# Kernel tuning notes

Measured on AMD Instinct MI355X. Metric: run time of the kernel, lower is better.

The kernel has to match this reference:

```python
import jax, jax.numpy as jnp
from jax import lax
import numpy as np

RANK, OUT_C, IN_C, K = 4, 128, 128, 3
B, H, W = 32, 56, 56


def setup_inputs() -> dict:
    key = jax.random.key(0)
    ks = jax.random.split(key, 7)
    x = jax.random.normal(ks[0], (B, IN_C, H, W), dtype=jnp.float32)
    # init_weights_normal per rank -> plain gaussian with fan-in scaling
    w = jax.random.normal(ks[1], (RANK, OUT_C, IN_C, K, K), dtype=jnp.float32) / np.sqrt(IN_C * K * K)
    cw_row = jax.random.normal(ks[2], (RANK, H, 1), dtype=jnp.float32) * 0.1
    cw_col = jax.random.normal(ks[3], (RANK, 1, W), dtype=jnp.float32) * 0.1
    b_row = jax.random.normal(ks[4], (1, 1, H, 1), dtype=jnp.float32) * 0.01
    b_col = jax.random.normal(ks[5], (1, 1, 1, W), dtype=jnp.float32) * 0.01
    b = jax.random.normal(ks[6], (1, OUT_C, 1, 1), dtype=jnp.float32) * 0.01
    return {"x": x, "w": w, "cw_row": cw_row, "cw_col": cw_col,
            "b_row": b_row, "b_col": b_col, "b": b}


def reference(x, w, cw_row, cw_col, b_row, b_col, b):
    # lrlc_nan branch: one big conv with rank*out_channels filters,
    # then per-spatial-location low-rank combining weights.
    rank, oc, ic, kh, kw = w.shape
    w_flat = w.reshape(rank * oc, ic, kh, kw)
    convs = lax.conv_general_dilated(
        x, w_flat,
        window_strides=(1, 1),
        padding=((1, 1), (1, 1)),
        dimension_numbers=("NCHW", "OIHW", "NCHW"),
    )  # [B, rank*oc, H, W]
    bsz = x.shape[0]
    hh, ww = convs.shape[2], convs.shape[3]
    convs = convs.reshape(bsz, rank, oc, hh, ww)
    # softmax over rank of per-location combining weights [rank, H, W]
    cw = jax.nn.softmax(cw_row + cw_col, axis=0)
    out = jnp.einsum("bkcxy,kxy->bcxy", convs, cw)
    # bias_pd: per-channel + per-row + per-col biases
    out = out + b + b_col + b_row
    return out
```

## Files before the change

### kernel.cpp

```cpp
#include <hip/hip_runtime.h>

#define NB 32
#define NC 128
#define NH 56
#define NW 56
#define HP 58
#define WP 58
#define KK 1152
#define NPOS 3136
#define XT_BYTES (NB * HP * WP * NC * 2)
#define AW_OFF XT_BYTES

typedef __attribute__((ext_vector_type(8))) short s16x8;
typedef __attribute__((ext_vector_type(4))) float f32x4;
typedef unsigned int u32;

__device__ __forceinline__ unsigned short f2bf(float f) {
    union { float f; unsigned int u; } v; v.f = f;
    unsigned int u = v.u + 0x7fffu + ((v.u >> 16) & 1u);
    return (unsigned short)(u >> 16);
}

__device__ __forceinline__ void gld16(const void* g, void* l) {
    __builtin_amdgcn_global_load_lds(
        (const __attribute__((address_space(1))) u32*)g,
        (__attribute__((address_space(3))) u32*)l, 16, 0, 0);
}

__global__ void k_xpose(const float* __restrict__ x, unsigned short* __restrict__ xt) {
    __shared__ unsigned short tile[128 * 57];
    int blk = blockIdx.x;
    int b = blk / NH, y = blk % NH;
    int tid = threadIdx.x;
    const float* xb = x + (size_t)b * (NC * NPOS) + y * NW;
#pragma unroll
    for (int p = 0; p < 7; ++p) {
        int idx = p * 256 + tid;
        int c = idx / 14, i = idx - c * 14;
        float4 v = *(const float4*)(xb + c * NPOS + i * 4);
        unsigned short* tp = &tile[c * 57 + i * 4];
        tp[0] = f2bf(v.x); tp[1] = f2bf(v.y); tp[2] = f2bf(v.z); tp[3] = f2bf(v.w);
    }
    __syncthreads();
    unsigned short* xrow = xt + ((size_t)(b * HP + y + 1) * WP + 1) * NC;
#pragma unroll
    for (int p = 0; p < 4; ++p) {
        int idx = p * 256 + tid;
        if (idx < 896) {
            int xp = idx >> 4, cgi = idx & 15;
            s16x8 v8;
#pragma unroll
            for (int j = 0; j < 8; ++j)
                v8[j] = (short)tile[(cgi * 8 + j) * 57 + xp];
            *(s16x8*)(xrow + xp * NC + cgi * 8) = v8;
        }
    }
    if (tid < 128) {
        xt[((size_t)(b * HP + y + 1) * WP + 0) * NC + tid] = 0;
        xt[((size_t)(b * HP + y + 1) * WP + 57) * NC + tid] = 0;
    }
    if (y == 0) {
        unsigned short* r0 = xt + (size_t)(b * HP + 0) * WP * NC;
        for (int i = tid; i < WP * NC; i += 256) r0[i] = 0;
    }
    if (y == 55) {
        unsigned short* r57 = xt + (size_t)(b * HP + 57) * WP * NC;
        for (int i = tid; i < WP * NC; i += 256) r57[i] = 0;
    }
}

__global__ void k_wconv(const float* __restrict__ w, unsigned short* __restrict__ aw) {
    int idx = blockIdx.x * 256 + threadIdx.x;
    if (idx >= 512 * KK) return;
    int j = idx & 7, lane = (idx >> 3) & 63, mt = (idx >> 9) & 31, s = idx >> 14;
    int m = mt * 16 + (lane & 15);
    int kg = s * 32 + (lane >> 4) * 8 + j;
    int g = kg >> 7, ic = kg & 127;
    aw[idx] = f2bf(w[(m * 128 + ic) * 9 + g]);
}

__global__ void __launch_bounds__(512, 2) k_main(
    const unsigned short* __restrict__ xt, const unsigned short* __restrict__ aw,
    const float* __restrict__ cwr, const float* __restrict__ cwc,
    const float* __restrict__ brow, const float* __restrict__ bcol,
    const float* __restrict__ bch, float* __restrict__ out) {
    __shared__ __align__(16) unsigned char ldsB[28672];

    const int tid = threadIdx.x;
    const int lane = tid & 63;
    const int wv = tid >> 6;
    const int l15 = lane & 15, quad = lane >> 4;
    const int blk = blockIdx.x;
    const int b = blk / 28;
    const int tile0 = (blk - b * 28) * 112;

    const unsigned char* gB0 = nullptr;
    const unsigned char* gB1 = nullptr;
    if (wv < 7) {
#pragma unroll
        for (int h = 0; h < 2; ++h) {
            int row = wv * 16 + h * 8 + (lane >> 3);
            int pos = tile0 + row;
            int yy = pos / 56, xx = pos - yy * 56;
            const unsigned char* p = (const unsigned char*)xt
                + (size_t)b * (HP * WP * NC * 2)
                + ((yy + 1) * WP + (xx + 1)) * (NC * 2)
                + (((lane & 7) ^ (lane >> 3)) * 16);
            if (h == 0) gB0 = p; else gB1 = p;
        }
    }

    const unsigned char* gA = (const unsigned char*)aw + wv * 1024 + lane * 16;

    s16x8 Areg[2][2][4];
    f32x4 acc[4][7] = {};

    auto aload = [&](int st, int set) {
#pragma unroll
        for (int kk = 0; kk < 2; ++kk)
#pragma unroll
            for (int r = 0; r < 4; ++r)
                Areg[set][kk][r] = *(const s16x8*)(gA + (((2 * st + kk) * 32 + r * 8) << 10));
    };

    auto bstage = [&](int st, int pbuf) {
        if (wv < 7) {
            int g = st >> 1;
            int dy = (g * 11) >> 5;
            int dx = g - dy * 3;
            int off = ((dy - 1) * WP + (dx - 1)) * (NC * 2) + (st & 1) * 128;
            unsigned char* L = ldsB + pbuf * 14336 + wv * 2048;
            gld16(gB0 + off, L);
            gld16(gB1 + off, L + 1024);
        }
    };

    bstage(0, 0);
    aload(0, 0);
    __syncthreads();

    for (int st = 0; st < 18; ++st) {
        const int cur = st & 1;
        if (st < 17) {
            bstage(st + 1, cur ^ 1);
            aload(st + 1, cur ^ 1);
        }
        const unsigned char* L = ldsB + cur * 14336;
#pragma unroll
        for (int kk = 0; kk < 2; ++kk) {
            s16x8 bf[7];
#pragma unroll
            for (int t = 0; t < 7; ++t)
                bf[t] = *(const s16x8*)(L + (t * 16 + l15) * 128
                                          + (((kk * 4 + quad) ^ (l15 & 7)) * 16));
#pragma unroll
            for (int r = 0; r < 4; ++r)
#pragma unroll
                for (int t = 0; t < 7; ++t)
                    acc[r][t] = __builtin_amdgcn_mfma_f32_16x16x32_bf16(
                        Areg[cur][kk][r], bf[t], acc[r][t], 0, 0, 0);
        }
        __syncthreads();
    }

#pragma unroll
    for (int t = 0; t < 7; ++t) {
        int pos = tile0 + t * 16 + l15;
        int yy = pos / 56, xx = pos - yy * 56;
        float v0 = cwr[yy]       + cwc[xx];
        float v1 = cwr[56 + yy]  + cwc[56 + xx];
        float v2 = cwr[112 + yy] + cwc[112 + xx];
        float v3 = cwr[168 + yy] + cwc[168 + xx];
        float mx = fmaxf(fmaxf(v0, v1), fmaxf(v2, v3));
        float e0 = __expf(v0 - mx), e1 = __expf(v1 - mx);
        float e2 = __expf(v2 - mx), e3 = __expf(v3 - mx);
        float inv = 1.0f / (e0 + e1 + e2 + e3);
        float c0 = e0 * inv, c1 = e1 * inv, c2 = e2 * inv, c3 = e3 * inv;
        float rb = brow[yy] + bcol[xx];
#pragma unroll
        for (int r = 0; r < 4; ++r) {
            int ch = wv * 16 + quad * 4 + r;
            float v = acc[0][t][r] * c0 + acc[1][t][r] * c1
                    + acc[2][t][r] * c2 + acc[3][t][r] * c3;
            out[((size_t)b * NC + ch) * NPOS + pos] = v + bch[ch] + rb;
        }
    }
}

extern "C" void kernel_launch(void* const* d_in, const int* in_sizes, int n_in,
                              void* d_out, int out_size, void* d_ws, size_t ws_size,
                              hipStream_t stream) {
    const float* x    = (const float*)d_in[0];
    const float* w    = (const float*)d_in[1];
    const float* cwr  = (const float*)d_in[2];
    const float* cwc  = (const float*)d_in[3];
    const float* brow = (const float*)d_in[4];
    const float* bcol = (const float*)d_in[5];
    const float* bch  = (const float*)d_in[6];
    float* out = (float*)d_out;

    unsigned char* ws = (unsigned char*)d_ws;
    unsigned short* xt = (unsigned short*)ws;
    unsigned short* aw = (unsigned short*)(ws + AW_OFF);

    k_xpose<<<NB * NH, 256, 0, stream>>>(x, xt);
    k_wconv<<<(512 * KK) / 256, 256, 0, stream>>>(w, aw);
    k_main<<<NB * 28, 512, 0, stream>>>(xt, aw, cwr, cwc, brow, bcol, bch, out);
}
```

Before: 251.7 us.

## Make each wave stage its own B tile and drop block barriers

Restructures k_main so each wave loads its own slice of the input tile into private LDS with global_load_lds. It then waits on vmcnt counters instead of a block-wide __syncthreads, with 36 finer K-stages double-buffered per wave. Waves are now split 4 (channel groups) by 2 (position halves, 4 or 3 N-tiles), each covering 32 output channels. This removes block barrier stalls and lets waves run independently. The cost is that the same B data is loaded redundantly by each of the 4 channel-group waves, LDS use doubles, and the hand-written vmcnt waits rely on the exact number of loads issued.

Measured after the change: 260.0 us. 3.3% more time.

```diff
diff --git a/kernel.cpp b/kernel.cpp
--- a/kernel.cpp
+++ b/kernel.cpp
@@ -79,93 +79,73 @@
     aw[idx] = f2bf(w[(m * 128 + ic) * 9 + g]);
 }
 
-__global__ void __launch_bounds__(512, 2) k_main(
-    const unsigned short* __restrict__ xt, const unsigned short* __restrict__ aw,
+template <int NT>
+__device__ __forceinline__ void wave_body(
+    const unsigned char* __restrict__ xt_b, const unsigned char* __restrict__ gA,
+    unsigned char* myL, int bufsz, int tile0, int nbase, int mg, int lane,
     const float* __restrict__ cwr, const float* __restrict__ cwc,
     const float* __restrict__ brow, const float* __restrict__ bcol,
-    const float* __restrict__ bch, float* __restrict__ out) {
-    __shared__ __align__(16) unsigned char ldsB[28672];
-
-    const int tid = threadIdx.x;
-    const int lane = tid & 63;
-    const int wv = tid >> 6;
+    const float* __restrict__ bch, float* __restrict__ out_b) {
     const int l15 = lane & 15, quad = lane >> 4;
-    const int blk = blockIdx.x;
-    const int b = blk / 28;
-    const int tile0 = (blk - b * 28) * 112;
-
-    const unsigned char* gB0 = nullptr;
-    const unsigned char* gB1 = nullptr;
-    if (wv < 7) {
-#pragma unroll
-        for (int h = 0; h < 2; ++h) {
-            int row = wv * 16 + h * 8 + (lane >> 3);
-            int pos = tile0 + row;
-            int yy = pos / 56, xx = pos - yy * 56;
-            const unsigned char* p = (const unsigned char*)xt
-                + (size_t)b * (HP * WP * NC * 2)
-                + ((yy + 1) * WP + (xx + 1)) * (NC * 2)
-                + (((lane & 7) ^ (lane >> 3)) * 16);
-            if (h == 0) gB0 = p; else gB1 = p;
-        }
-    }
-
-    const unsigned char* gA = (const unsigned char*)aw + wv * 1024 + lane * 16;
+
+    const unsigned char* gB[NT];
+#pragma unroll
+    for (int i = 0; i < NT; ++i) {
+        int row = i * 16 + (lane >> 2);
+        int pos = tile0 + nbase + row;
+        int yy = pos / 56, xx = pos - yy * 56;
+        int lc = (lane & 3) ^ ((lane >> 3) & 3);
+        gB[i] = xt_b + ((yy + 1) * WP + (xx + 1)) * (NC * 2) + lc * 16;
+    }
+    const int b_base = l15 * 64 + ((quad ^ ((l15 >> 1) & 3)) * 16);
 
     s16x8 Areg[2][2][4];
-    f32x4 acc[4][7] = {};
-
-    auto aload = [&](int st, int set) {
-#pragma unroll
-        for (int kk = 0; kk < 2; ++kk)
+    f32x4 acc[2][4][NT] = {};
+
+    auto issue = [&](int st, int buf) {
+        int g = st >> 2;
+        int dy = (g * 11) >> 5, dx = g - dy * 3;
+        int off = ((dy - 1) * WP + (dx - 1)) * (NC * 2) + (st & 3) * 64;
+        unsigned char* L = myL + buf * bufsz;
+#pragma unroll
+        for (int i = 0; i < NT; ++i) gld16(gB[i] + off, L + i * 1024);
+#pragma unroll
+        for (int h = 0; h < 2; ++h)
 #pragma unroll
             for (int r = 0; r < 4; ++r)
-                Areg[set][kk][r] = *(const s16x8*)(gA + (((2 * st + kk) * 32 + r * 8) << 10));
+                Areg[buf][h][r] = *(const s16x8*)(gA + st * 32768 + h * 1024 + r * 8192);
     };
-
-    auto bstage = [&](int st, int pbuf) {
-        if (wv < 7) {
-            int g = st >> 1;
-            int dy = (g * 11) >> 5;
-            int dx = g - dy * 3;
-            int off = ((dy - 1) * WP + (dx - 1)) * (NC * 2) + (st & 1) * 128;
-            unsigned char* L = ldsB + pbuf * 14336 + wv * 2048;
-            gld16(gB0 + off, L);
-            gld16(gB1 + off, L + 1024);
-        }
+    auto waitNV = [&]() {
+        if constexpr (NT == 4) asm volatile("s_waitcnt vmcnt(12)" ::: "memory");
+        else                   asm volatile("s_waitcnt vmcnt(11)" ::: "memory");
     };
-
-    bstage(0, 0);
-    aload(0, 0);
-    __syncthreads();
-
-    for (int st = 0; st < 18; ++st) {
-        const int cur = st & 1;
-        if (st < 17) {
-            bstage(st + 1, cur ^ 1);
-            aload(st + 1, cur ^ 1);
-        }
-        const unsigned char* L = ldsB + cur * 14336;
-#pragma unroll
-        for (int kk = 0; kk < 2; ++kk) {
-            s16x8 bf[7];
-#pragma unroll
-            for (int t = 0; t < 7; ++t)
-                bf[t] = *(const s16x8*)(L + (t * 16 + l15) * 128
-                                          + (((kk * 4 + quad) ^ (l15 & 7)) * 16));
+    auto compute = [&](int buf) {
+        const unsigned char* L = myL + buf * bufsz;
+        s16x8 bf[NT];
+#pragma unroll
+        for (int t = 0; t < NT; ++t) bf[t] = *(const s16x8*)(L + t * 1024 + b_base);
+#pragma unroll
+        for (int h = 0; h < 2; ++h)
 #pragma unroll
             for (int r = 0; r < 4; ++r)
 #pragma unroll
-                for (int t = 0; t < 7; ++t)
-                    acc[r][t] = __builtin_amdgcn_mfma_f32_16x16x32_bf16(
-                        Areg[cur][kk][r], bf[t], acc[r][t], 0, 0, 0);
-        }
-        __syncthreads();
-    }
-
-#pragma unroll
-    for (int t = 0; t < 7; ++t) {
-        int pos = tile0 + t * 16 + l15;
+                for (int t = 0; t < NT; ++t)
+                    acc[h][r][t] = __builtin_amdgcn_mfma_f32_16x16x32_bf16(
+                        Areg[buf][h][r], bf[t], acc[h][r][t], 0, 0, 0);
+    };
+
+    issue(0, 0);
+    for (int s = 0; s < 34; s += 2) {
+        issue(s + 1, 1); waitNV(); compute(0);
+        issue(s + 2, 0); waitNV(); compute(1);
+    }
+    issue(35, 1); waitNV(); compute(0);
+    asm volatile("s_waitcnt vmcnt(0)" ::: "memory");
+    compute(1);
+
+#pragma unroll
+    for (int t = 0; t < NT; ++t) {
+        int pos = tile0 + nbase + t * 16 + l15;
         int yy = pos / 56, xx = pos - yy * 56;
         float v0 = cwr[yy]       + cwc[xx];
         float v1 = cwr[56 + yy]  + cwc[56 + xx];
@@ -178,13 +158,43 @@
         float c0 = e0 * inv, c1 = e1 * inv, c2 = e2 * inv, c3 = e3 * inv;
         float rb = brow[yy] + bcol[xx];
 #pragma unroll
-        for (int r = 0; r < 4; ++r) {
-            int ch = wv * 16 + quad * 4 + r;
-            float v = acc[0][t][r] * c0 + acc[1][t][r] * c1
-                    + acc[2][t][r] * c2 + acc[3][t][r] * c3;
-            out[((size_t)b * NC + ch) * NPOS + pos] = v + bch[ch] + rb;
-        }
-    }
+        for (int h = 0; h < 2; ++h)
+#pragma unroll
+            for (int r = 0; r < 4; ++r) {
+                int ch = (2 * mg + h) * 16 + quad * 4 + r;
+                float v = acc[h][0][t][r] * c0 + acc[h][1][t][r] * c1
+                        + acc[h][2][t][r] * c2 + acc[h][3][t][r] * c3;
+                out_b[(size_t)ch * NPOS + pos] = v + bch[ch] + rb;
+            }
+    }
+}
+
+__global__ void __launch_bounds__(512, 2) k_main(
+    const unsigned short* __restrict__ xt, const unsigned short* __restrict__ aw,
+    const float* __restrict__ cwr, const float* __restrict__ cwc,
+    const float* __restrict__ brow, const float* __restrict__ bcol,
+    const float* __restrict__ bch, float* __restrict__ out) {
+    __shared__ __align__(16) unsigned char ldsB[57344];
+
+    const int tid = threadIdx.x;
+    const int lane = tid & 63;
+    const int wv = tid >> 6;
+    const int mg = wv >> 1, ng = wv & 1;
+    const int blk = blockIdx.x;
+    const int b = blk / 28;
+    const int tile0 = (blk - b * 28) * 112;
+
+    const unsigned char* xt_b = (const unsigned char*)xt + (size_t)b * (HP * WP * NC * 2);
+    const unsigned char* gA = (const unsigned char*)aw + (2 * mg) * 1024 + lane * 16;
+    unsigned char* myL = ldsB + mg * 14336 + ng * 8192;
+    float* out_b = out + (size_t)b * NC * NPOS;
+
+    if (ng == 0)
+        wave_body<4>(xt_b, gA, myL, 4096, tile0, 0, mg, lane,
+                     cwr, cwc, brow, bcol, bch, out_b);
+    else
+        wave_body<3>(xt_b, gA, myL, 3072, tile0, 64, mg, lane,
+                     cwr, cwc, brow, bcol, bch, out_b);
 }
 
 extern "C" void kernel_launch(void* const* d_in, const int* in_sizes, int n_in,
```

## Merge prologue kernels and widen main-loop K stages to full channel slices

Applied to the files above, without the earlier changes.

The input transpose and weight conversion kernels are merged into one launch, with block ranges split by index, which saves a kernel launch and lets the two prologue jobs overlap. The main GEMM loop now stages a full 128-channel slice per filter tap (9 stages instead of 18) into a 2x28 KB LDS double buffer with an XOR swizzle over 16 chunks. A-fragment register prefetch moves to a finer per-kk ping-pong. The change halves the number of barriers and raises the LDS footprint, which may lower occupancy at two blocks per CU.

Result: faster. 234.1 us (-7.0%).

```diff
diff --git a/kernel.cpp b/kernel.cpp
--- a/kernel.cpp
+++ b/kernel.cpp
@@ -27,11 +27,23 @@
         (__attribute__((address_space(3))) u32*)l, 16, 0, 0);
 }
 
-__global__ void k_xpose(const float* __restrict__ x, unsigned short* __restrict__ xt) {
+__global__ void k_pro(const float* __restrict__ x, const float* __restrict__ w,
+                      unsigned short* __restrict__ xt, unsigned short* __restrict__ aw) {
+    int blk = blockIdx.x;
+    int tid = threadIdx.x;
+    if (blk >= 1792) {
+        int idx = (blk - 1792) * 256 + tid;
+        if (idx < 512 * KK) {
+            int j = idx & 7, lane = (idx >> 3) & 63, mt = (idx >> 9) & 31, s = idx >> 14;
+            int m = mt * 16 + (lane & 15);
+            int kg = s * 32 + (lane >> 4) * 8 + j;
+            int g = kg >> 7, ic = kg & 127;
+            aw[idx] = f2bf(w[(m * 128 + ic) * 9 + g]);
+        }
+        return;
+    }
     __shared__ unsigned short tile[128 * 57];
-    int blk = blockIdx.x;
     int b = blk / NH, y = blk % NH;
-    int tid = threadIdx.x;
     const float* xb = x + (size_t)b * (NC * NPOS) + y * NW;
 #pragma unroll
     for (int p = 0; p < 7; ++p) {
@@ -69,22 +81,12 @@
     }
 }
 
-__global__ void k_wconv(const float* __restrict__ w, unsigned short* __restrict__ aw) {
-    int idx = blockIdx.x * 256 + threadIdx.x;
-    if (idx >= 512 * KK) return;
-    int j = idx & 7, lane = (idx >> 3) & 63, mt = (idx >> 9) & 31, s = idx >> 14;
-    int m = mt * 16 + (lane & 15);
-    int kg = s * 32 + (lane >> 4) * 8 + j;
-    int g = kg >> 7, ic = kg & 127;
-    aw[idx] = f2bf(w[(m * 128 + ic) * 9 + g]);
-}
-
 __global__ void __launch_bounds__(512, 2) k_main(
     const unsigned short* __restrict__ xt, const unsigned short* __restrict__ aw,
     const float* __restrict__ cwr, const float* __restrict__ cwc,
     const float* __restrict__ brow, const float* __restrict__ bcol,
     const float* __restrict__ bch, float* __restrict__ out) {
-    __shared__ __align__(16) unsigned char ldsB[28672];
+    __shared__ __align__(16) unsigned char ldsB[2][28672];
 
     const int tid = threadIdx.x;
     const int lane = tid & 63;
@@ -94,71 +96,63 @@
     const int b = blk / 28;
     const int tile0 = (blk - b * 28) * 112;
 
-    const unsigned char* gB0 = nullptr;
-    const unsigned char* gB1 = nullptr;
+    const unsigned char* xt_b = (const unsigned char*)xt + (size_t)b * (HP * WP * NC * 2);
+    const unsigned char* gA = (const unsigned char*)aw + wv * 1024 + lane * 16;
+
+    const unsigned char* gB[4];
     if (wv < 7) {
 #pragma unroll
-        for (int h = 0; h < 2; ++h) {
-            int row = wv * 16 + h * 8 + (lane >> 3);
+        for (int h = 0; h < 4; ++h) {
+            int rl = h * 4 + (lane >> 4);
+            int row = wv * 16 + rl;
             int pos = tile0 + row;
             int yy = pos / 56, xx = pos - yy * 56;
-            const unsigned char* p = (const unsigned char*)xt
-                + (size_t)b * (HP * WP * NC * 2)
-                + ((yy + 1) * WP + (xx + 1)) * (NC * 2)
-                + (((lane & 7) ^ (lane >> 3)) * 16);
-            if (h == 0) gB0 = p; else gB1 = p;
-        }
-    }
-
-    const unsigned char* gA = (const unsigned char*)aw + wv * 1024 + lane * 16;
-
-    s16x8 Areg[2][2][4];
+            int c = (lane & 15) ^ rl;
+            gB[h] = xt_b + ((yy + 1) * WP + (xx + 1)) * (NC * 2) + c * 16;
+        }
+    }
+
+    s16x8 Areg[2][4];
     f32x4 acc[4][7] = {};
 
-    auto aload = [&](int st, int set) {
-#pragma unroll
-        for (int kk = 0; kk < 2; ++kk)
-#pragma unroll
-            for (int r = 0; r < 4; ++r)
-                Areg[set][kk][r] = *(const s16x8*)(gA + (((2 * st + kk) * 32 + r * 8) << 10));
+    auto aload = [&](int s32, int pp) {
+#pragma unroll
+        for (int r = 0; r < 4; ++r)
+            Areg[pp][r] = *(const s16x8*)(gA + s32 * 32768 + r * 8192);
     };
-
-    auto bstage = [&](int st, int pbuf) {
+    auto bissue = [&](int st, int buf) {
         if (wv < 7) {
-            int g = st >> 1;
-            int dy = (g * 11) >> 5;
-            int dx = g - dy * 3;
-            int off = ((dy - 1) * WP + (dx - 1)) * (NC * 2) + (st & 1) * 128;
-            unsigned char* L = ldsB + pbuf * 14336 + wv * 2048;
-            gld16(gB0 + off, L);
-            gld16(gB1 + off, L + 1024);
+            int dy = (st * 11) >> 5, dx = st - dy * 3;
+            int off = ((dy - 1) * WP + (dx - 1)) * (NC * 2);
+            unsigned char* L = &ldsB[buf][wv * 4096];
+#pragma unroll
+            for (int h = 0; h < 4; ++h) gld16(gB[h] + off, L + h * 1024);
         }
     };
 
-    bstage(0, 0);
     aload(0, 0);
+    bissue(0, 0);
     __syncthreads();
 
-    for (int st = 0; st < 18; ++st) {
+    for (int st = 0; st < 9; ++st) {
         const int cur = st & 1;
-        if (st < 17) {
-            bstage(st + 1, cur ^ 1);
-            aload(st + 1, cur ^ 1);
-        }
-        const unsigned char* L = ldsB + cur * 14336;
-#pragma unroll
-        for (int kk = 0; kk < 2; ++kk) {
+        if (st < 8) bissue(st + 1, cur ^ 1);
+        const unsigned char* L = &ldsB[cur][0];
+#pragma unroll
+        for (int kk = 0; kk < 4; ++kk) {
+            if (kk < 3) aload(st * 4 + kk + 1, (kk + 1) & 1);
+            else if (st < 8) aload((st + 1) * 4, 0);
             s16x8 bf[7];
 #pragma unroll
             for (int t = 0; t < 7; ++t)
-                bf[t] = *(const s16x8*)(L + (t * 16 + l15) * 128
-                                          + (((kk * 4 + quad) ^ (l15 & 7)) * 16));
+                bf[t] = *(const s16x8*)(L + (t * 16 + l15) * 256
+                                          + (((kk * 4 + quad) ^ l15) << 4));
 #pragma unroll
             for (int r = 0; r < 4; ++r)
 #pragma unroll
                 for (int t = 0; t < 7; ++t)
                     acc[r][t] = __builtin_amdgcn_mfma_f32_16x16x32_bf16(
-                        Areg[cur][kk][r], bf[t], acc[r][t], 0, 0, 0);
+                        Areg[kk & 1][r], bf[t], acc[r][t], 0, 0, 0);
         }
         __syncthreads();
     }
@@ -203,7 +197,6 @@
     unsigned short* xt = (unsigned short*)ws;
     unsigned short* aw = (unsigned short*)(ws + AW_OFF);
 
-    k_xpose<<<NB * NH, 256, 0, stream>>>(x, xt);
-    k_wconv<<<(512 * KK) / 256, 256, 0, stream>>>(w, aw);
+    k_pro<<<4096, 256, 0, stream>>>(x, w, xt, aw);
     k_main<<<NB * 28, 512, 0, stream>>>(xt, aw, cwr, cwc, brow, bcol, bch, out);
 }
```
